# Kernel optimization log

Hardware: AMD Instinct MI355X
Metric: run time of the kernel (lower is better)

## Reference

```python
import jax, jax.numpy as jnp
import numpy as np

CHANNELS = 512
GROUPS = 32
EPS = 1e-5


def setup_inputs() -> dict:
    key = jax.random.key(0)
    ks = jax.random.split(key, 7)
    C = CHANNELS
    x = jax.random.normal(ks[0], (32, C, 32, 32), dtype=jnp.float32)
    norm_w = jax.random.normal(ks[1], (C,), dtype=jnp.float32) * 0.02 + 1.0
    norm_b = jax.random.normal(ks[2], (C,), dtype=jnp.float32) * 0.02
    # 1x1 convs stored as (out_channels, in_channels)
    qkv_w = jax.random.normal(ks[3], (3 * C, C), dtype=jnp.float32) * (C ** -0.5)
    qkv_b = jax.random.normal(ks[4], (3 * C,), dtype=jnp.float32) * 0.02
    proj_w = jax.random.normal(ks[5], (C, C), dtype=jnp.float32) * (C ** -0.5)
    proj_b = jax.random.normal(ks[6], (C,), dtype=jnp.float32) * 0.02
    return {"x": x, "norm_w": norm_w, "norm_b": norm_b,
            "qkv_w": qkv_w, "qkv_b": qkv_b,
            "proj_w": proj_w, "proj_b": proj_b}


def _group_norm(x, w, b):
    B, C, H, W = x.shape
    xg = x.reshape(B, GROUPS, C // GROUPS, H, W)
    mean = xg.mean(axis=(2, 3, 4), keepdims=True)
    var = xg.var(axis=(2, 3, 4), keepdims=True)
    xn = ((xg - mean) * jax.lax.rsqrt(var + EPS)).reshape(B, C, H, W)
    return xn * w[None, :, None, None] + b[None, :, None, None]


def reference(x, norm_w, norm_b, qkv_w, qkv_b, proj_w, proj_b):
    B, C, H, W = x.shape
    scale = C ** (-0.5)
    h = _group_norm(x, norm_w, norm_b)
    # 1x1 conv == per-pixel linear: (B,C,H,W) -> (B,3C,H,W)
    qkv = jnp.einsum('bchw,oc->bohw', h, qkv_w) + qkv_b[None, :, None, None]
    qkv = qkv.reshape(B, 3, C, H * W)
    q, k, v = qkv[:, 0], qkv[:, 1], qkv[:, 2]  # each (B, C, N)
    # attn[b, i, j] = softmax_j( q[:, i] . k[:, j] * scale )
    scores = jnp.einsum('bcn,bcm->bnm', q, k) * scale  # (B, N, N)
    attn = jax.nn.softmax(scores, axis=-1)
    # h[b, c, i] = sum_j v[b, c, j] * attn[b, i, j]
    hout = jnp.einsum('bcm,bnm->bcn', v, attn).reshape(B, C, H, W)
    out = x + jnp.einsum('bchw,oc->bohw', hout, proj_w) + proj_b[None, :, None, None]
    return out
```

## Files before the change

kernel.cpp:

```cpp
#include <hip/hip_runtime.h>
#include <math.h>

#define B_ 32
#define C_ 512
#define G_ 32
#define N_ 1024
#define OC3_ 1536
#define EPS_ 1e-5f

typedef __attribute__((ext_vector_type(8))) short short8;
typedef __attribute__((ext_vector_type(4))) float f32x4;

__device__ inline unsigned short f2bf(float f) {
    unsigned u = __builtin_bit_cast(unsigned, f);
    u += 0x7fffu + ((u >> 16) & 1u);
    return (unsigned short)(u >> 16);
}
__device__ inline unsigned pack2(float lo, float hi) {
    return (unsigned)f2bf(lo) | ((unsigned)f2bf(hi) << 16);
}
__device__ inline float bf2f(unsigned short u) {
    return __builtin_bit_cast(float, ((unsigned)u) << 16);
}

typedef const __attribute__((address_space(1))) unsigned int* gas_u32;
typedef __attribute__((address_space(3))) unsigned int* las_u32;
__device__ __forceinline__ void cp16(unsigned short* lds, const unsigned short* g) {
    __builtin_amdgcn_global_load_lds((gas_u32)g, (las_u32)lds, 16, 0, 0);
}

__global__ __launch_bounds__(256) void gn_stats_kernel(
    const float* __restrict__ x, float* __restrict__ stats)
{
    int bg = blockIdx.x;
    const float4* xv = (const float4*)(x + (size_t)bg * 16 * N_);
    float s = 0.f, ss = 0.f;
    for (int i = threadIdx.x; i < 4096; i += 256) {
        float4 v = xv[i];
        s  += v.x + v.y + v.z + v.w;
        ss += v.x*v.x + v.y*v.y + v.z*v.z + v.w*v.w;
    }
    __shared__ float r1[256], r2[256];
    r1[threadIdx.x] = s; r2[threadIdx.x] = ss;
    __syncthreads();
    for (int off = 128; off > 0; off >>= 1) {
        if (threadIdx.x < off) {
            r1[threadIdx.x] += r1[threadIdx.x + off];
            r2[threadIdx.x] += r2[threadIdx.x + off];
        }
        __syncthreads();
    }
    if (threadIdx.x == 0) {
        float mean = r1[0] * (1.f / 16384.f);
        float var  = r2[0] * (1.f / 16384.f) - mean * mean;
        stats[bg * 2 + 0] = mean;
        stats[bg * 2 + 1] = rsqrtf(var + EPS_);
    }
}

__global__ __launch_bounds__(256) void cvt_bf16_kernel(
    const float* __restrict__ src, unsigned short* __restrict__ dst, int n4)
{
    int i = blockIdx.x * 256 + threadIdx.x;
    if (i >= n4) return;
    float4 v = ((const float4*)src)[i];
    uint2 o; o.x = pack2(v.x, v.y); o.y = pack2(v.z, v.w);
    ((uint2*)dst)[i] = o;
}

__global__ __launch_bounds__(256) void hhatT_kernel(
    const float* __restrict__ x, const float* __restrict__ stats,
    const float* __restrict__ nw, const float* __restrict__ nbias,
    unsigned short* __restrict__ hhatT, long sH, int b0)
{
    int bz = blockIdx.z, b = b0 + bz;
    int nt = blockIdx.x * 64, ct = blockIdx.y * 64;
    const float* xb = x + (size_t)b * C_ * N_;
    const float* st = stats + b * 2 * G_;

    __shared__ float T[64][65];
    int tid = threadIdx.x;

    #pragma unroll
    for (int p = 0; p < 4; ++p) {
        int c = p * 16 + (tid >> 4);
        int n4 = (tid & 15) * 4;
        float4 v = *(const float4*)&xb[(size_t)(ct + c) * N_ + nt + n4];
        int g = (ct + c) >> 4;
        float w0 = nw[ct + c] * st[g * 2 + 1];
        float bb = nbias[ct + c] - st[g * 2] * w0;
        T[c][n4]   = v.x * w0 + bb;
        T[c][n4+1] = v.y * w0 + bb;
        T[c][n4+2] = v.z * w0 + bb;
        T[c][n4+3] = v.w * w0 + bb;
    }
    __syncthreads();
    #pragma unroll
    for (int p = 0; p < 2; ++p) {
        int n  = p * 32 + (tid >> 3);
        int c8 = (tid & 7) * 8;
        short8 s;
        #pragma unroll
        for (int u = 0; u < 8; ++u) s[u] = (short)f2bf(T[c8 + u][n]);
        *(short8*)&hhatT[(size_t)bz * sH + (size_t)(nt + n) * C_ + ct + c8] = s;
    }
}

template<int EPI>
__global__ __launch_bounds__(256) void gemm128(
    const unsigned short* __restrict__ A, long sA, int lda,
    const unsigned short* __restrict__ B, long sB, int ldb,
    void* __restrict__ Dv, long sD, int ldd,
    const float* __restrict__ bias,
    const float* __restrict__ aux, long sAux,
    int K, float scale, int gx, int gy, int nbz)
{
    int bid = blockIdx.x;
    int nbpb = gx * gy;
    int bx, by, bz;
    if ((nbz & 7) == 0) {
        int xcd = bid & 7;
        int rest = bid >> 3;
        int local = rest % nbpb;
        int bg = rest / nbpb;
        bz = bg * 8 + xcd;
        bx = local % gx;
        by = local / gx;
    } else {
        bz = bid / nbpb;
        int local = bid % nbpb;
        bx = local % gx;
        by = local / gx;
    }

    const unsigned short* Ab = A + (size_t)bz * sA + (size_t)bx * 128 * lda;
    const unsigned short* Bb = B + (size_t)bz * sB + (size_t)by * 128 * ldb;

    __shared__ __align__(16) unsigned short smem[4][4096];

    int tid = threadIdx.x;
    int w = tid >> 6, lane = tid & 63;
    int lm = lane & 15, q = lane >> 4;
    int wrow = (w >> 1) * 64, wcol = (w & 1) * 64;

    f32x4 acc[4][4];
    #pragma unroll
    for (int i = 0; i < 4; ++i)
        #pragma unroll
        for (int j = 0; j < 4; ++j) acc[i][j] = (f32x4)(0.f);

    int srow = tid >> 2;
    int skc  = (((tid & 3) ^ ((tid >> 3) & 3))) * 8;
    int fco  = (q ^ ((lm >> 1) & 3)) * 8;

    const unsigned short* a0p = Ab + (size_t)srow        * lda + skc;
    const unsigned short* a1p = Ab + (size_t)(64 + srow) * lda + skc;
    const unsigned short* b0p = Bb + (size_t)srow        * ldb + skc;
    const unsigned short* b1p = Bb + (size_t)(64 + srow) * ldb + skc;

    cp16(&smem[0][tid * 8],        a0p);
    cp16(&smem[0][2048 + tid * 8], a1p);
    cp16(&smem[2][tid * 8],        b0p);
    cp16(&smem[2][2048 + tid * 8], b1p);

    int nIter = K >> 5;
    for (int it = 0; it < nIter; ++it) {
        int cur = it & 1;
        __syncthreads();
        if (it + 1 < nIter) {
            int off = (it + 1) * 32;
            int nxt = cur ^ 1;
            cp16(&smem[nxt][tid * 8],            a0p + off);
            cp16(&smem[nxt][2048 + tid * 8],     a1p + off);
            cp16(&smem[2 + nxt][tid * 8],        b0p + off);
            cp16(&smem[2 + nxt][2048 + tid * 8], b1p + off);
        }
        short8 af[4], bf[4];
        #pragma unroll
        for (int i = 0; i < 4; ++i)
            af[i] = *(const short8*)&smem[cur][(wrow + i * 16 + lm) * 32 + fco];
        #pragma unroll
        for (int j = 0; j < 4; ++j)
            bf[j] = *(const short8*)&smem[2 + cur][(wcol + j * 16 + lm) * 32 + fco];
        #pragma unroll
        for (int i = 0; i < 4; ++i)
            #pragma unroll
            for (int j = 0; j < 4; ++j)
                acc[i][j] = __builtin_amdgcn_mfma_f32_16x16x32_bf16(
                    af[i], bf[j], acc[i][j], 0, 0, 0);
    }

    __syncthreads();

    if constexpr (EPI != 4) {
        unsigned short* Ts = &smem[0][0];
        #pragma unroll
        for (int j = 0; j < 4; ++j) {
            int lc = wcol + j * 16 + lm;
            float cb = (EPI == 0) ? bias[by * 128 + lc] : 0.f;
            #pragma unroll
            for (int i = 0; i < 4; ++i) {
                #pragma unroll
                for (int r = 0; r < 4; ++r) {
                    int lr = wrow + i * 16 + q * 4 + r;
                    float vle = acc[i][j][r];
                    if constexpr (EPI == 0) vle += cb;
                    else if constexpr (EPI == 1) vle += bias[bx * 128 + lr];
                    else if constexpr (EPI == 2) vle *= scale;
                    Ts[lr * 128 + (lc ^ (q << 3))] = f2bf(vle);
                }
            }
        }
        __syncthreads();
        unsigned short* Dp = (unsigned short*)Dv +
            (size_t)bz * sD + (size_t)(bx * 128) * ldd + by * 128;
        #pragma unroll
        for (int k = 0; k < 8; ++k) {
            int flat = k * 2048 + tid * 8;
            int rr = flat >> 7, cc = flat & 127;
            int key = (rr >> 2) & 3;
            short8 vv = *(const short8*)&Ts[flat ^ (key << 3)];
            *(short8*)&Dp[(size_t)rr * ldd + cc] = vv;
        }
    } else {
        float* Ts32 = (float*)&smem[0][0];
        float* Dp = (float*)Dv + (size_t)bz * sD + (size_t)(bx * 128) * ldd + by * 128;
        const float* Ap = aux + (size_t)bz * sAux + (size_t)(bx * 128) * ldd + by * 128;
        #pragma unroll
        for (int h = 0; h < 2; ++h) {
            if (h) __syncthreads();
            if ((w & 1) == h) {
                #pragma unroll
                for (int j = 0; j < 4; ++j) {
                    int lch = j * 16 + lm;
                    #pragma unroll
                    for (int i = 0; i < 4; ++i) {
                        #pragma unroll
                        for (int r = 0; r < 4; ++r) {
                            int lr = wrow + i * 16 + q * 4 + r;
                            Ts32[lr * 64 + (lch ^ (q << 3))] =
                                acc[i][j][r] + bias[bx * 128 + lr];
                        }
                    }
                }
            }
            __syncthreads();
            #pragma unroll
            for (int k = 0; k < 8; ++k) {
                int flat = k * 1024 + tid * 4;
                int rr = flat >> 6, cc = flat & 63;
                int key = (rr >> 2) & 3;
                f32x4 vv = *(const f32x4*)&Ts32[flat ^ (key << 3)];
                size_t go = (size_t)rr * ldd + h * 64 + cc;
                f32x4 av = *(const f32x4*)&Ap[go];
                *(f32x4*)&Dp[go] = vv + av;
            }
        }
    }
}

__global__ __launch_bounds__(256) void softmax_kernel(
    unsigned short* __restrict__ sc, long sSc)
{
    int bz = blockIdx.y;
    int row = blockIdx.x * 4 + (threadIdx.x >> 6);
    int lane = threadIdx.x & 63;
    unsigned short* p = sc + (size_t)bz * sSc + (size_t)row * N_ + lane * 16;

    short8 s0 = *(const short8*)p;
    short8 s1 = *(const short8*)(p + 8);
    float v[16];
    #pragma unroll
    for (int i = 0; i < 8; ++i) {
        v[i]     = bf2f((unsigned short)s0[i]);
        v[8 + i] = bf2f((unsigned short)s1[i]);
    }
    float m = v[0];
    #pragma unroll
    for (int i = 1; i < 16; ++i) m = fmaxf(m, v[i]);
    #pragma unroll
    for (int off = 32; off > 0; off >>= 1) m = fmaxf(m, __shfl_xor(m, off, 64));

    float sum = 0.f;
    #pragma unroll
    for (int i = 0; i < 16; ++i) { v[i] = __expf(v[i] - m); sum += v[i]; }
    #pragma unroll
    for (int off = 32; off > 0; off >>= 1) sum += __shfl_xor(sum, off, 64);
    float inv = 1.f / sum;

    short8 o0, o1;
    #pragma unroll
    for (int i = 0; i < 8; ++i) {
        o0[i] = (short)f2bf(v[i] * inv);
        o1[i] = (short)f2bf(v[8 + i] * inv);
    }
    *(short8*)p = o0;
    *(short8*)(p + 8) = o1;
}

extern "C" void kernel_launch(void* const* d_in, const int* in_sizes, int n_in,
                              void* d_out, int out_size, void* d_ws, size_t ws_size,
                              hipStream_t stream) {
    const float* x      = (const float*)d_in[0];
    const float* norm_w = (const float*)d_in[1];
    const float* norm_b = (const float*)d_in[2];
    const float* qkv_w  = (const float*)d_in[3];
    const float* qkv_b  = (const float*)d_in[4];
    const float* proj_w = (const float*)d_in[5];
    const float* proj_b = (const float*)d_in[6];
    float* out = (float*)d_out;

    char* ws = (char*)d_ws;
    float* stats = (float*)ws;
    unsigned short* wqkv  = (unsigned short*)(ws + 8192);
    unsigned short* wproj = wqkv + (size_t)OC3_ * C_;
    char* base = (char*)(wproj + (size_t)C_ * C_);
    const size_t fixed = 8192 + (size_t)OC3_ * C_ * 2 + (size_t)C_ * C_ * 2;

    const size_t REG = 6u << 20;
    const long RSH = (long)(REG / 2);

    size_t avail = ws_size > fixed ? ws_size - fixed : 0;
    int chunk = (int)(avail / REG);
    if (chunk < 1) chunk = 1;
    if (chunk > B_) chunk = B_;

    gn_stats_kernel<<<dim3(B_ * G_), dim3(256), 0, stream>>>(x, stats);
    cvt_bf16_kernel<<<dim3((OC3_ * C_ / 4 + 255) / 256), dim3(256), 0, stream>>>(
        qkv_w, wqkv, OC3_ * C_ / 4);
    cvt_bf16_kernel<<<dim3((C_ * C_ / 4 + 255) / 256), dim3(256), 0, stream>>>(
        proj_w, wproj, C_ * C_ / 4);

    const float scale = 0.044194173824159216f;

    unsigned short* qkT   = (unsigned short*)base;
    unsigned short* vbuf  = (unsigned short*)(base + (2u << 20));
    unsigned short* hhatT = (unsigned short*)(base + (3u << 20));
    unsigned short* houtT = (unsigned short*)(base + (3u << 20));
    unsigned short* sc    = (unsigned short*)(base + (4u << 20));

    for (int b0 = 0; b0 < B_; b0 += chunk) {
        int nb = B_ - b0 < chunk ? B_ - b0 : chunk;

        hhatT_kernel<<<dim3(N_/64, C_/64, nb), dim3(256), 0, stream>>>(
            x, stats, norm_w, norm_b, hhatT, RSH, b0);

        gemm128<0><<<dim3(8 * 8 * nb), dim3(256), 0, stream>>>(
            hhatT, RSH, C_,  wqkv, 0, C_,
            qkT, RSH, 1024,  qkv_b, nullptr, 0, C_, 0.f, 8, 8, nb);

        gemm128<1><<<dim3(4 * 8 * nb), dim3(256), 0, stream>>>(
            wqkv + (size_t)1024 * C_, 0, C_,  hhatT, RSH, C_,
            vbuf, RSH, N_,  qkv_b + 1024, nullptr, 0, C_, 0.f, 4, 8, nb);

        gemm128<2><<<dim3(8 * 8 * nb), dim3(256), 0, stream>>>(
            qkT, RSH, 1024,  qkT + 512, RSH, 1024,
            sc, RSH, N_,  nullptr, nullptr, 0, C_, scale, 8, 8, nb);

        softmax_kernel<<<dim3(N_/4, nb), dim3(256), 0, stream>>>(sc, RSH);

        gemm128<3><<<dim3(8 * 4 * nb), dim3(256), 0, stream>>>(
            sc, RSH, N_,  vbuf, RSH, N_,
            houtT, RSH, C_,  nullptr, nullptr, 0, N_, 0.f, 8, 4, nb);

        gemm128<4><<<dim3(4 * 8 * nb), dim3(256), 0, stream>>>(
            wproj, 0, C_,  houtT, RSH, C_,
            out + (size_t)b0 * C_ * N_, (long)C_ * N_, N_,
            proj_b, x + (size_t)b0 * C_ * N_, (long)C_ * N_, C_, 0.f, 4, 8, nb);
    }
}
```

Measured before the change: 382.4 us.

## Merge QK and V projection GEMMs into one launch, XCD-aware block mapping

Combines the QK projection GEMM and the transposed V projection GEMM into a single gemm128<5> launch, using the block index to select which sub-problem each block computes. hhatT and softmax kernels now use the same XCD-aware batch decode as the GEMMs. The LDS epilogue swizzle is widened from 4 to 8 keys to reduce bank conflicts. This saves a launch and a tail, but adds branching in address and bias selection and relies on a hardcoded 1<<20 offset for vbuf.

```diff
diff --git a/kernel.cpp b/kernel.cpp
--- a/kernel.cpp
+++ b/kernel.cpp
@@ -27,6 +27,19 @@
 typedef __attribute__((address_space(3))) unsigned int* las_u32;
 __device__ __forceinline__ void cp16(unsigned short* lds, const unsigned short* g) {
     __builtin_amdgcn_global_load_lds((gas_u32)g, (las_u32)lds, 16, 0, 0);
+}
+
+__device__ __forceinline__ void xcd_decode(int bid, int nbpb, int nbz,
+                                           int& bz, int& local) {
+    if ((nbz & 7) == 0) {
+        int xcd = bid & 7;
+        int rest = bid >> 3;
+        local = rest % nbpb;
+        bz = (rest / nbpb) * 8 + xcd;
+    } else {
+        bz = bid / nbpb;
+        local = bid % nbpb;
+    }
 }
 
 __global__ __launch_bounds__(256) void gn_stats_kernel(
@@ -71,10 +84,12 @@
 __global__ __launch_bounds__(256) void hhatT_kernel(
     const float* __restrict__ x, const float* __restrict__ stats,
     const float* __restrict__ nw, const float* __restrict__ nbias,
-    unsigned short* __restrict__ hhatT, long sH, int b0)
-{
-    int bz = blockIdx.z, b = b0 + bz;
-    int nt = blockIdx.x * 64, ct = blockIdx.y * 64;
+    unsigned short* __restrict__ hhatT, long sH, int b0, int nbz)
+{
+    int bz, local;
+    xcd_decode(blockIdx.x, 128, nbz, bz, local);
+    int b = b0 + bz;
+    int nt = (local & 15) * 64, ct = (local >> 4) * 64;
     const float* xb = x + (size_t)b * C_ * N_;
     const float* st = stats + b * 2 * G_;
 
@@ -115,26 +130,34 @@
     const float* __restrict__ aux, long sAux,
     int K, float scale, int gx, int gy, int nbz)
 {
-    int bid = blockIdx.x;
-    int nbpb = gx * gy;
-    int bx, by, bz;
-    if ((nbz & 7) == 0) {
-        int xcd = bid & 7;
-        int rest = bid >> 3;
-        int local = rest % nbpb;
-        int bg = rest / nbpb;
-        bz = bg * 8 + xcd;
+    int bz, local;
+    xcd_decode(blockIdx.x, gx * gy, nbz, bz, local);
+
+    int bx, by;
+    bool p2 = false;
+    if constexpr (EPI == 5) {
+        p2 = local >= 64;
+        int li = p2 ? local - 64 : local;
+        bx = p2 ? (li & 3) : (li & 7);
+        by = p2 ? (li >> 2) : (li >> 3);
+    } else {
         bx = local % gx;
         by = local / gx;
+    }
+
+    const unsigned short *Ab, *Bb;
+    if constexpr (EPI == 5) {
+        if (p2) {
+            Ab = B + (size_t)(1024 + bx * 128) * ldb;
+            Bb = A + (size_t)bz * sA + (size_t)by * 128 * lda;
+        } else {
+            Ab = A + (size_t)bz * sA + (size_t)bx * 128 * lda;
+            Bb = B + (size_t)by * 128 * ldb;
+        }
     } else {
-        bz = bid / nbpb;
-        int local = bid % nbpb;
-        bx = local % gx;
-        by = local / gx;
-    }
-
-    const unsigned short* Ab = A + (size_t)bz * sA + (size_t)bx * 128 * lda;
-    const unsigned short* Bb = B + (size_t)bz * sB + (size_t)by * 128 * ldb;
+        Ab = A + (size_t)bz * sA + (size_t)bx * 128 * lda;
+        Bb = B + (size_t)bz * sB + (size_t)by * 128 * ldb;
+    }
 
     __shared__ __align__(16) unsigned short smem[4][4096];
 
@@ -197,28 +220,32 @@
         #pragma unroll
         for (int j = 0; j < 4; ++j) {
             int lc = wcol + j * 16 + lm;
-            float cb = (EPI == 0) ? bias[by * 128 + lc] : 0.f;
+            float cb = 0.f;
+            if constexpr (EPI == 5) { if (!p2) cb = bias[by * 128 + lc]; }
             #pragma unroll
             for (int i = 0; i < 4; ++i) {
                 #pragma unroll
                 for (int r = 0; r < 4; ++r) {
                     int lr = wrow + i * 16 + q * 4 + r;
                     float vle = acc[i][j][r];
-                    if constexpr (EPI == 0) vle += cb;
-                    else if constexpr (EPI == 1) vle += bias[bx * 128 + lr];
-                    else if constexpr (EPI == 2) vle *= scale;
-                    Ts[lr * 128 + (lc ^ (q << 3))] = f2bf(vle);
+                    if constexpr (EPI == 2) vle *= scale;
+                    else if constexpr (EPI == 5)
+                        vle += p2 ? bias[1024 + bx * 128 + lr] : cb;
+                    int wkey = (lr >> 2) & 7;
+                    Ts[lr * 128 + (lc ^ (wkey << 3))] = f2bf(vle);
                 }
             }
         }
         __syncthreads();
-        unsigned short* Dp = (unsigned short*)Dv +
+        size_t doff = 0;
+        if constexpr (EPI == 5) { if (p2) doff = (size_t)(1u << 20); }
+        unsigned short* Dp = (unsigned short*)Dv + doff +
             (size_t)bz * sD + (size_t)(bx * 128) * ldd + by * 128;
         #pragma unroll
         for (int k = 0; k < 8; ++k) {
             int flat = k * 2048 + tid * 8;
             int rr = flat >> 7, cc = flat & 127;
-            int key = (rr >> 2) & 3;
+            int key = (rr >> 2) & 7;
             short8 vv = *(const short8*)&Ts[flat ^ (key << 3)];
             *(short8*)&Dp[(size_t)rr * ldd + cc] = vv;
         }
@@ -238,7 +265,8 @@
                         #pragma unroll
                         for (int r = 0; r < 4; ++r) {
                             int lr = wrow + i * 16 + q * 4 + r;
-                            Ts32[lr * 64 + (lch ^ (q << 3))] =
+                            int wkey = (lr >> 2) & 7;
+                            Ts32[lr * 64 + (lch ^ (wkey << 3))] =
                                 acc[i][j][r] + bias[bx * 128 + lr];
                         }
                     }
@@ -249,7 +277,7 @@
             for (int k = 0; k < 8; ++k) {
                 int flat = k * 1024 + tid * 4;
                 int rr = flat >> 6, cc = flat & 63;
-                int key = (rr >> 2) & 3;
+                int key = (rr >> 2) & 7;
                 f32x4 vv = *(const f32x4*)&Ts32[flat ^ (key << 3)];
                 size_t go = (size_t)rr * ldd + h * 64 + cc;
                 f32x4 av = *(const f32x4*)&Ap[go];
@@ -260,10 +288,11 @@
 }
 
 __global__ __launch_bounds__(256) void softmax_kernel(
-    unsigned short* __restrict__ sc, long sSc)
-{
-    int bz = blockIdx.y;
-    int row = blockIdx.x * 4 + (threadIdx.x >> 6);
+    unsigned short* __restrict__ sc, long sSc, int nbz)
+{
+    int bz, local;
+    xcd_decode(blockIdx.x, 256, nbz, bz, local);
+    int row = local * 4 + (threadIdx.x >> 6);
     int lane = threadIdx.x & 63;
     unsigned short* p = sc + (size_t)bz * sSc + (size_t)row * N_ + lane * 16;
 
@@ -342,22 +371,18 @@
     for (int b0 = 0; b0 < B_; b0 += chunk) {
         int nb = B_ - b0 < chunk ? B_ - b0 : chunk;
 
-        hhatT_kernel<<<dim3(N_/64, C_/64, nb), dim3(256), 0, stream>>>(
-            x, stats, norm_w, norm_b, hhatT, RSH, b0);
-
-        gemm128<0><<<dim3(8 * 8 * nb), dim3(256), 0, stream>>>(
+        hhatT_kernel<<<dim3(128 * nb), dim3(256), 0, stream>>>(
+            x, stats, norm_w, norm_b, hhatT, RSH, b0, nb);
+
+        gemm128<5><<<dim3(96 * nb), dim3(256), 0, stream>>>(
             hhatT, RSH, C_,  wqkv, 0, C_,
-            qkT, RSH, 1024,  qkv_b, nullptr, 0, C_, 0.f, 8, 8, nb);
-
-        gemm128<1><<<dim3(4 * 8 * nb), dim3(256), 0, stream>>>(
-            wqkv + (size_t)1024 * C_, 0, C_,  hhatT, RSH, C_,
-            vbuf, RSH, N_,  qkv_b + 1024, nullptr, 0, C_, 0.f, 4, 8, nb);
+            qkT, RSH, 1024,  qkv_b, nullptr, 0, C_, 0.f, 96, 1, nb);
 
         gemm128<2><<<dim3(8 * 8 * nb), dim3(256), 0, stream>>>(
             qkT, RSH, 1024,  qkT + 512, RSH, 1024,
             sc, RSH, N_,  nullptr, nullptr, 0, C_, scale, 8, 8, nb);
 
-        softmax_kernel<<<dim3(N_/4, nb), dim3(256), 0, stream>>>(sc, RSH);
+        softmax_kernel<<<dim3(256 * nb), dim3(256), 0, stream>>>(sc, RSH, nb);
 
         gemm128<3><<<dim3(8 * 4 * nb), dim3(256), 0, stream>>>(
             sc, RSH, N_,  vbuf, RSH, N_,
```

After: 385.2 us. No clear change (+0.7%).
